# Performance work log

Measured on AMD Instinct MI355X. Metric: run time of the kernel, lower is better.

Reference implementation:

```python
import jax, jax.numpy as jnp
import numpy as np
from jax import lax

B, T, V, LAT, U, P = 256, 128, 42, 200, 512, 3  # batch, seq, vocab, latent, lstm units, num_prop


def setup_inputs() -> dict:
    key = jax.random.key(0)
    ks = jax.random.split(key, 40)
    g = lambda i, shape, s=0.05: (jax.random.normal(ks[i], shape, jnp.float32) * s)
    inp = {
        'X': jax.random.randint(ks[0], (B, T), 0, V, jnp.int64 if jax.config.jax_enable_x64 else jnp.int32),
        'Y': jax.random.randint(ks[1], (B, T), 0, V, jnp.int32),
        'C': jax.random.normal(ks[2], (B, P), jnp.float32),
        'L': jax.random.randint(ks[3], (B,), 1, T + 1, jnp.int32),
        'eps': jax.random.normal(ks[4], (B, LAT), jnp.float32),
        'emb_enc': g(5, (V, LAT), 0.1),
        'emb_dec': g(6, (V, LAT), 0.1),
        # encoder stacked LSTM: layer0 input dim = LAT + P, layers 1-2 input dim = U
        'enc_k0': g(7, (LAT + P, 4 * U)), 'enc_rk0': g(8, (U, 4 * U)), 'enc_b0': jnp.zeros((4 * U,), jnp.float32),
        'enc_k1': g(9, (U, 4 * U)), 'enc_rk1': g(10, (U, 4 * U)), 'enc_b1': jnp.zeros((4 * U,), jnp.float32),
        'enc_k2': g(11, (U, 4 * U)), 'enc_rk2': g(12, (U, 4 * U)), 'enc_b2': jnp.zeros((4 * U,), jnp.float32),
        # decoder stacked LSTM: layer0 input dim = 2*LAT + P
        'dec_k0': g(13, (2 * LAT + P, 4 * U)), 'dec_rk0': g(14, (U, 4 * U)), 'dec_b0': jnp.zeros((4 * U,), jnp.float32),
        'dec_k1': g(15, (U, 4 * U)), 'dec_rk1': g(16, (U, 4 * U)), 'dec_b1': jnp.zeros((4 * U,), jnp.float32),
        'dec_k2': g(17, (U, 4 * U)), 'dec_rk2': g(18, (U, 4 * U)), 'dec_b2': jnp.zeros((4 * U,), jnp.float32),
        'Wm': g(19, (U, LAT)), 'bm': jnp.zeros((LAT,), jnp.float32),
        'Ws': g(20, (U, LAT)), 'bs': jnp.zeros((LAT,), jnp.float32),
        'Wo': g(21, (U, V)), 'bo': jnp.zeros((V,), jnp.float32),
    }
    return inp


def _lstm_step(x, h, c, k, rk, b):
    # Keras LSTMCell gate order: i, f, g(candidate), o
    z = x @ k + h @ rk + b
    i, f, gg, o = jnp.split(z, 4, axis=-1)
    c2 = jax.nn.sigmoid(f) * c + jax.nn.sigmoid(i) * jnp.tanh(gg)
    h2 = jax.nn.sigmoid(o) * jnp.tanh(c2)
    return h2, c2


def _run_stacked(inp, params):
    # inp: [B, T, D]; params: list of 3 (kernel, recurrent_kernel, bias)
    b = inp.shape[0]
    init = tuple((jnp.zeros((b, U), inp.dtype), jnp.zeros((b, U), inp.dtype)) for _ in range(3))

    def scan_fn(carry, x_t):
        h_in = x_t
        new = []
        for (h, c), (k, rk, bb) in zip(carry, params):
            h2, c2 = _lstm_step(h_in, h, c, k, rk, bb)
            new.append((h2, c2))
            h_in = h2
        return tuple(new), h_in

    carry, ys = lax.scan(scan_fn, init, jnp.swapaxes(inp, 0, 1))
    return jnp.swapaxes(ys, 0, 1), carry  # [B,T,U], final states


def reference(X, Y, C, L, eps, emb_enc, emb_dec,
              enc_k0, enc_rk0, enc_b0, enc_k1, enc_rk1, enc_b1, enc_k2, enc_rk2, enc_b2,
              dec_k0, dec_rk0, dec_b0, dec_k1, dec_rk1, dec_b1, dec_k2, dec_rk2, dec_b2,
              Wm, bm, Ws, bs, Wo, bo):
    enc_params = [(enc_k0, enc_rk0, enc_b0), (enc_k1, enc_rk1, enc_b1), (enc_k2, enc_rk2, enc_b2)]
    dec_params = [(dec_k0, dec_rk0, dec_b0), (dec_k1, dec_rk1, dec_b1), (dec_k2, dec_rk2, dec_b2)]

    # ---- encode ----
    Xe = emb_enc[X]                                       # [B,T,LAT]
    Ct = jnp.broadcast_to(C[:, None, :], (B, T, P))
    enc_in = jnp.concatenate([Xe, Ct], axis=-1)           # [B,T,LAT+P]
    _, enc_states = _run_stacked(enc_in, enc_params)
    h = enc_states[-1][1]                                 # CELL state of last layer (state[-1][1])
    mean = h @ Wm + bm
    log_sigma = h @ Ws + bs
    z = mean + jnp.exp(log_sigma / 2.0) * eps             # [B,LAT]

    # ---- decode ----
    Zt = jnp.broadcast_to(z[:, None, :], (B, T, LAT))
    Xd = emb_dec[X]
    dec_in = jnp.concatenate([Zt, Xd, Ct], axis=-1)       # [B,T,2*LAT+P]
    dec_out, _ = _run_stacked(dec_in, dec_params)
    pre = dec_out @ Wo + bo                               # pre-softmax logits [B,T,V]

    # ---- losses ----
    logp = jax.nn.log_softmax(pre, axis=-1)
    ce = -jnp.take_along_axis(logp, Y[..., None].astype(jnp.int32), axis=-1)[..., 0]  # [B,T]
    weights = (jnp.arange(T)[None, :] < L[:, None]).astype(jnp.float32)
    recon = jnp.mean(ce * weights)
    latent = -0.5 * jnp.mean(1.0 + log_sigma - jnp.square(mean) - jnp.exp(log_sigma))
    loss = recon + latent
    return loss, recon, latent
```

## Files before the change

### kernel.cpp

```cpp
#include <hip/hip_runtime.h>

#define B_ 256
#define T_ 128
#define V_ 42
#define LAT_ 200
#define U_ 512
#define G4_ 2048
#define NBLK 196
#define FI(r, m) ((((r) * 2) + (m)) * 32)
#define SLOT_ ((size_t)B_ * U_)
#define LS_ ((size_t)129 * SLOT_)

typedef unsigned short ushort_t;
typedef __attribute__((ext_vector_type(8))) short bf8;
typedef __attribute__((ext_vector_type(4))) float f4;

__device__ __forceinline__ ushort_t f2bf(float f) {
  union { float f; unsigned int i; } v; v.f = f;
  unsigned int r = v.i + 0x7fffu + ((v.i >> 16) & 1u);
  return (ushort_t)(r >> 16);
}
__device__ __forceinline__ float sigf(float x) { return 1.f / (1.f + __expf(-x)); }
__device__ __forceinline__ float tanhfast(float x) {
  float e = __expf(2.f * x);
  return 1.f - 2.f / (e + 1.f);
}

__device__ __forceinline__ void st_wt_b16(void* p, ushort_t v) {
  unsigned int vv = v;
  asm volatile("global_store_short %0, %1, off sc0 sc1" :: "v"(p), "v"(vv) : "memory");
}
__device__ __forceinline__ void st_wt_b32(void* p, unsigned int v) {
  asm volatile("global_store_dword %0, %1, off sc0 sc1" :: "v"(p), "v"(v) : "memory");
}
__device__ __forceinline__ void wait_vm0() {
  asm volatile("s_waitcnt vmcnt(0)" ::: "memory");
}

__global__ __launch_bounds__(256) void table_kernel(const float* emb, const float* k0, int roff, float* table) {
  int v = blockIdx.x, tid = threadIdx.x;
  __shared__ float e[LAT_];
  for (int i = tid; i < LAT_; i += 256) e[i] = emb[v * LAT_ + i];
  __syncthreads();
  for (int j = tid; j < G4_; j += 256) {
    float s = 0.f;
    for (int n = 0; n < LAT_; n++) s += e[n] * k0[(size_t)(roff + n) * G4_ + j];
    table[v * G4_ + j] = s;
  }
}

__device__ __forceinline__ size_t mat_off_u4(int m) {
  if (m == 0) return 0;
  if (m == 1) return 147456;
  if (m < 10) return 360448 + (size_t)(m - 2) * 131072;
  return 1409024;
}

struct SwzSrc {
  const float *enc_rk0, *enc_k0, *enc_b0;
  const float *dec_rk0, *dec_k0, *dec_b0;
  const float *tabE, *tabD;
  const float *encK1, *encR1, *encK2, *encR2;
  const float *decK1, *decR1, *decK2, *decR2;
  const float *Wo;
  ushort_t* dst;
};

__device__ float swz_val(const SwzSrc& s, int mat, int k, int n) {
  switch (mat) {
    case 0: {
      if (k < 512) return s.enc_rk0[(size_t)k * G4_ + n];
      int i = k - 512;
      if (i < 42) return s.tabE[(size_t)i * G4_ + n];
      if (i < 45) return s.enc_k0[(size_t)(200 + i - 42) * G4_ + n];
      if (i == 45) return s.enc_b0[n];
      return 0.f;
    }
    case 1: {
      if (k < 512) return s.dec_rk0[(size_t)k * G4_ + n];
      int i = k - 512;
      if (i < 200) return s.dec_k0[(size_t)i * G4_ + n];
      if (i < 256) return 0.f;
      i -= 256;
      if (i < 42) return s.tabD[(size_t)i * G4_ + n];
      if (i < 45) return s.dec_k0[(size_t)(400 + i - 42) * G4_ + n];
      if (i == 45) return s.dec_b0[n];
      return 0.f;
    }
    case 2: return s.encK1[(size_t)k * G4_ + n];
    case 3: return s.encR1[(size_t)k * G4_ + n];
    case 4: return s.encK2[(size_t)k * G4_ + n];
    case 5: return s.encR2[(size_t)k * G4_ + n];
    case 6: return s.decK1[(size_t)k * G4_ + n];
    case 7: return s.decR1[(size_t)k * G4_ + n];
    case 8: return s.decK2[(size_t)k * G4_ + n];
    case 9: return s.decR2[(size_t)k * G4_ + n];
    default: return (n < V_) ? s.Wo[(size_t)k * V_ + n] : 0.f;
  }
}

__global__ __launch_bounds__(256) void swz_ext_kernel(SwzSrc s) {
  int b = blockIdx.x, tid = threadIdx.x;
  int mat, nt16;
  if (b < 1280) { mat = b >> 7; nt16 = b & 127; } else { mat = 10; nt16 = b - 1280; }
  int ktMax = (mat == 0) ? 18 : (mat == 1) ? 26 : 16;
  int lane = tid & 63, l15 = lane & 15, q = lane >> 4;
  int n = nt16 * 16 + l15;
  uint4* dst = (uint4*)s.dst;
  size_t off = mat_off_u4(mat);
  for (int kt = tid >> 6; kt < ktMax; kt += 4) {
    ushort_t o[8];
    int kb = kt * 32 + q * 8;
#pragma unroll
    for (int j = 0; j < 8; j++) o[j] = f2bf(swz_val(s, mat, kb + j, n));
    dst[off + ((size_t)nt16 * ktMax + kt) * 64 + lane] = *(const uint4*)o;
  }
}

struct PP {
  const ushort_t* swz;
  ushort_t* ring;
  float* c2g; ushort_t* zf16; float* sums; int* bar; int* gen; int* flg; float* out;
  const float *enc_b1, *enc_b2, *dec_b1, *dec_b2;
  const float *Wm, *bm, *Ws, *bs, *eps, *C, *bo;
  const int *X, *Y, *Lb;
};

__device__ __forceinline__ void grid_barrier(int* bar, int* gen) {
  __builtin_amdgcn_fence(__ATOMIC_RELEASE, "agent");
  __syncthreads();
  if (threadIdx.x == 0) {
    int g = __hip_atomic_load(gen, __ATOMIC_RELAXED, __HIP_MEMORY_SCOPE_AGENT);
    if (__hip_atomic_fetch_add(bar, 1, __ATOMIC_ACQ_REL, __HIP_MEMORY_SCOPE_AGENT) == NBLK - 1) {
      __hip_atomic_store(bar, 0, __ATOMIC_RELAXED, __HIP_MEMORY_SCOPE_AGENT);
      __hip_atomic_store(gen, g + 1, __ATOMIC_RELEASE, __HIP_MEMORY_SCOPE_AGENT);
    } else {
      int gg;
      do {
        __builtin_amdgcn_s_sleep(1);
        gg = __hip_atomic_load(gen, __ATOMIC_ACQUIRE, __HIP_MEMORY_SCOPE_AGENT);
      } while (gg == g);
    }
  }
  __syncthreads();
  __builtin_amdgcn_fence(__ATOMIC_ACQUIRE, "agent");
}

__device__ __forceinline__ void wait_flags(const int* f, int cnt, int target) {
  int lane = threadIdx.x & 63;
  const int* a = f + (lane < cnt ? lane : 0);
  bool bad;
  do {
    int v = __hip_atomic_load(a, __ATOMIC_RELAXED, __HIP_MEMORY_SCOPE_AGENT);
    bad = (lane < cnt) && (v < target);
    if (__ballot(bad) == 0ull) break;
    __builtin_amdgcn_s_sleep(1);
  } while (true);
}

#define MFMA(a, bfrag, c) __builtin_amdgcn_mfma_f32_16x16x32_bf16((a), (bfrag), (c), 0, 0, 0)

__global__ __launch_bounds__(256, 1) void persist(PP p) {
  __shared__ uint4 wlds4[8192];
  const int b = blockIdx.x, tid = threadIdx.x;
  const int lane = tid & 63, w = tid >> 6, q = lane >> 4, l15 = lane & 15;
  const int role = b < 64 ? 0 : b < 128 ? 1 : b < 192 ? 2 : 3;
  const int idx = b & 63;
  const int ut = idx >> 1;
  const int mi = idx & 1;
  const int m0 = mi * 128;
  const int rw = m0 + w * 32;
  const int u = ut * 16 + l15;
  const uint4* swzU4 = (const uint4*)p.swz;
  const int cb = b - 192;

  unsigned char* tok = (unsigned char*)wlds4 + 106496;
  unsigned char* ytok = (unsigned char*)wlds4 + 49152;

  ushort_t cb0[2][3];
  if (role == 0) {
#pragma unroll
    for (int ms = 0; ms < 2; ms++)
#pragma unroll
      for (int j = 0; j < 3; j++) cb0[ms][j] = f2bf(p.C[(rw + ms * 16 + l15) * 3 + j]);
  }

  const int pubidx = FI(role, mi) + ut;

  float ce_local = 0.f;
  float boR0 = 0.f, boR1 = 0.f, boR2 = 0.f;
  int Lr[4] = {0, 0, 0, 0};
  int pub = 0;

  for (int phase = 0; phase < 2; phase++) {
    const bool dec = (phase == 1);

    if (dec) {
      grid_barrier(p.bar, p.gen);
      if (b < 50) {
        int lat0 = b * 4;
        int row = tid;
        float m[4], ls[4];
#pragma unroll
        for (int lc = 0; lc < 4; lc++) { m[lc] = p.bm[lat0 + lc]; ls[lc] = p.bs[lat0 + lc]; }
        const float* cr = p.c2g + (size_t)row * U_;
        for (int k = 0; k < U_; k++) {
          float hv = cr[k];
#pragma unroll
          for (int lc = 0; lc < 4; lc++) {
            m[lc] += hv * p.Wm[k * LAT_ + lat0 + lc];
            ls[lc] += hv * p.Ws[k * LAT_ + lat0 + lc];
          }
        }
        float kl = 0.f;
#pragma unroll
        for (int lc = 0; lc < 4; lc++) {
          int lat = lat0 + lc;
          float zz = m[lc] + __expf(0.5f * ls[lc]) * p.eps[row * LAT_ + lat];
          p.zf16[row * 256 + lat] = f2bf(zz);
          kl += 1.f + ls[lc] - m[lc] * m[lc] - __expf(ls[lc]);
        }
        float* red = (float*)wlds4;
        red[tid] = kl; __syncthreads();
        for (int st = 128; st > 0; st >>= 1) { if (tid < st) red[tid] += red[tid + st]; __syncthreads(); }
        if (tid == 0) atomicAdd(p.sums + 1, red[0]);
      }
      __syncthreads();
    }

    const int KT = dec ? 26 : 18;
    if (role == 0) {
      int mat = dec ? 1 : 0;
      size_t mo = mat_off_u4(mat);
      for (int g = 0; g < 4; g++) {
        int nt16 = g * 32 + ut;
        size_t src = mo + (size_t)nt16 * KT * 64;
        int dst = g * KT * 64;
        for (int i = tid; i < KT * 64; i += 256) wlds4[dst + i] = swzU4[src + i];
      }
      if (!dec) {
        for (int i = tid; i < 128 * T_; i += 256) {
          int r = i >> 7, t = i & 127;
          tok[r * 133 + t] = (unsigned char)p.X[(size_t)(m0 + r) * T_ + t];
        }
      }
    } else if (role <= 2) {
      int matK = dec ? (role == 1 ? 6 : 8) : (role == 1 ? 2 : 4);
      for (int gm = 0; gm < 2; gm++) {
        size_t mo = mat_off_u4(matK + gm);
        for (int g = 0; g < 4; g++) {
          int nt16 = g * 32 + ut;
          size_t src = mo + (size_t)nt16 * 1024;
          int dst = gm * 4096 + g * 1024;
          for (int i = tid; i < 1024; i += 256) wlds4[dst + i] = swzU4[src + i];
        }
      }
    } else if (dec) {
      size_t mo = mat_off_u4(10);
      for (int i = tid; i < 3072; i += 256) wlds4[i] = swzU4[mo + i];
      for (int i = tid; i < 64 * T_; i += 256) {
        int r = i >> 7, t = i & 127;
        ytok[r * 133 + t] = (unsigned char)p.Y[(size_t)(cb * 64 + r) * T_ + t];
      }
      int r0c = cb * 64 + w * 16;
      boR0 = p.bo[l15]; boR1 = p.bo[16 + l15]; boR2 = (l15 < 10) ? p.bo[32 + l15] : 0.f;
#pragma unroll
      for (int r = 0; r < 4; r++) Lr[r] = p.Lb[r0c + q * 4 + r];
    }
    __syncthreads();

    float creg[2][4];
#pragma unroll
    for (int ms = 0; ms < 2; ms++)
#pragma unroll
      for (int r = 0; r < 4; r++) creg[ms][r] = 0.f;
    float bias[4] = {0.f, 0.f, 0.f, 0.f};
    if (role == 1 || role == 2) {
      const float* bb = dec ? (role == 1 ? p.dec_b1 : p.dec_b2) : (role == 1 ? p.enc_b1 : p.enc_b2);
#pragma unroll
      for (int g = 0; g < 4; g++) bias[g] = bb[g * 512 + u];
    }

    const int* myp = nullptr; int myc = 0;
    if (role == 0) {
      if (w == 0) { myp = p.flg + FI(0, mi); myc = 32; }
    } else if (role == 1) {
      if (w == 0) { myp = p.flg + FI(0, mi); myc = 32; }
      else if (w == 1) { myp = p.flg + FI(1, mi); myc = 32; }
    } else if (role == 2) {
      if (w == 0) { myp = p.flg + FI(1, mi); myc = 32; }
      else if (w == 1) { myp = p.flg + FI(2, mi); myc = 32; }
    } else {
      if (w == 0 && dec) { myp = p.flg + FI(2, cb >> 1); myc = 32; }
    }

    grid_barrier(p.bar, p.gen);

    bf8 zr0[8], zr1[8];
    if (role == 0 && dec) {
      const ushort_t* Az0 = p.zf16 + (rw + l15) * 256 + q * 8;
#pragma unroll
      for (int kz = 0; kz < 8; kz++) {
        zr0[kz] = *(const bf8*)(Az0 + kz * 32);
        zr1[kz] = *(const bf8*)(Az0 + 16 * 256 + kz * 32);
      }
    }

    const int smax = dec ? T_ + 3 : T_ + 2;
    for (int s = 0; s < smax; s++) {
      pub++;
      if (myc) wait_flags(myp, myc, pub - 1);
      __syncthreads();

      const int lag = (role <= 2) ? role : 3;
      const int t = s - lag;
      if (role == 3) {
        if (dec && t >= 0 && t < T_) {
          int r0c = cb * 64 + w * 16;
          const ushort_t* Ar = p.ring + 2 * LS_ + (size_t)(t + 1) * SLOT_ + (size_t)(r0c + l15) * U_ + q * 8;
          f4 a3[3];
#pragma unroll
          for (int nt = 0; nt < 3; nt++) a3[nt] = (f4){0.f, 0.f, 0.f, 0.f};
#pragma unroll 4
          for (int kt = 0; kt < 16; kt++) {
            bf8 a = *(const bf8*)(Ar + kt * 32);
#pragma unroll
            for (int nt = 0; nt < 3; nt++) {
              bf8 bbf = *(const bf8*)&wlds4[nt * 1024 + kt * 64 + lane];
              a3[nt] = MFMA(a, bbf, a3[nt]);
            }
          }
#pragma unroll
          for (int r = 0; r < 4; r++) {
            float v0 = a3[0][r] + boR0;
            float v1 = a3[1][r] + boR1;
            float v2 = (l15 < 10) ? a3[2][r] + boR2 : -3.0e38f;
            float mx = fmaxf(fmaxf(v0, v1), v2);
            mx = fmaxf(mx, __shfl_xor(mx, 1)); mx = fmaxf(mx, __shfl_xor(mx, 2));
            mx = fmaxf(mx, __shfl_xor(mx, 4)); mx = fmaxf(mx, __shfl_xor(mx, 8));
            float se = __expf(v0 - mx) + __expf(v1 - mx) + ((l15 < 10) ? __expf(v2 - mx) : 0.f);
            int yv = ytok[(w * 16 + q * 4 + r) * 133 + t];
            float py = (l15 == yv ? v0 : 0.f) + (l15 + 16 == yv ? v1 : 0.f) + (l15 + 32 == yv ? v2 : 0.f);
            se += __shfl_xor(se, 1); se += __shfl_xor(se, 2); se += __shfl_xor(se, 4); se += __shfl_xor(se, 8);
            py += __shfl_xor(py, 1); py += __shfl_xor(py, 2); py += __shfl_xor(py, 4); py += __shfl_xor(py, 8);
            if (l15 == 0 && t < Lr[r]) ce_local += mx + __logf(se) - py;
          }
        }
      } else if (t >= 0 && t < T_) {
        f4 acc[2][4];
#pragma unroll
        for (int ms = 0; ms < 2; ms++)
#pragma unroll
          for (int g = 0; g < 4; g++) acc[ms][g] = (f4){0.f, 0.f, 0.f, 0.f};

        const ushort_t* hin = p.ring + (size_t)role * LS_ + (size_t)t * SLOT_;
        ushort_t* hout = p.ring + (size_t)role * LS_ + (size_t)(t + 1) * SLOT_;
        const ushort_t* Ah0 = hin + (size_t)(rw + l15) * U_ + q * 8;
        const ushort_t* Ah1 = Ah0 + 16 * U_;

        if (role == 0) {
          const int KT64 = KT * 64;
#pragma unroll 4
          for (int kt = 0; kt < 16; kt++) {
            bf8 a0 = *(const bf8*)(Ah0 + kt * 32);
            bf8 a1 = *(const bf8*)(Ah1 + kt * 32);
#pragma unroll
            for (int g = 0; g < 4; g++) {
              bf8 bbf = *(const bf8*)&wlds4[g * KT64 + kt * 64 + lane];
              acc[0][g] = MFMA(a0, bbf, acc[0][g]);
              acc[1][g] = MFMA(a1, bbf, acc[1][g]);
            }
          }
          if (dec) {
#pragma unroll
            for (int kz = 0; kz < 8; kz++) {
#pragma unroll
              for (int g = 0; g < 4; g++) {
                bf8 bbf = *(const bf8*)&wlds4[g * KT64 + (16 + kz) * 64 + lane];
                acc[0][g] = MFMA(zr0[kz], bbf, acc[0][g]);
                acc[1][g] = MFMA(zr1[kz], bbf, acc[1][g]);
              }
            }
          }
          int xv0 = tok[(w * 32 + l15) * 133 + t];
          int xv1 = tok[(w * 32 + 16 + l15) * 133 + t];
#pragma unroll
          for (int ktc = 0; ktc < 2; ktc++) {
            union { ushort_t us[8]; bf8 v; } a0u, a1u;
#pragma unroll
            for (int j = 0; j < 8; j++) {
              int id = ktc * 32 + q * 8 + j;
              ushort_t v0 = (id == xv0) ? (ushort_t)0x3F80 : (ushort_t)0;
              ushort_t v1 = (id == xv1) ? (ushort_t)0x3F80 : (ushort_t)0;
              if (id >= 42 && id < 45) { v0 = cb0[0][id - 42]; v1 = cb0[1][id - 42]; }
              if (id == 45) { v0 = 0x3F80; v1 = 0x3F80; }
              a0u.us[j] = v0; a1u.us[j] = v1;
            }
            int kt = KT - 2 + ktc;
#pragma unroll
            for (int g = 0; g < 4; g++) {
              bf8 bbf = *(const bf8*)&wlds4[g * KT64 + kt * 64 + lane];
              acc[0][g] = MFMA(a0u.v, bbf, acc[0][g]);
              acc[1][g] = MFMA(a1u.v, bbf, acc[1][g]);
            }
          }
        } else {
          const ushort_t* xin = p.ring + (size_t)(role - 1) * LS_ + (size_t)(t + 1) * SLOT_;
          const ushort_t* Ax0 = xin + (size_t)(rw + l15) * U_ + q * 8;
          const ushort_t* Ax1 = Ax0 + 16 * U_;
#pragma unroll 4
          for (int kt = 0; kt < 16; kt++) {
            bf8 a0 = *(const bf8*)(Ax0 + kt * 32);
            bf8 a1 = *(const bf8*)(Ax1 + kt * 32);
#pragma unroll
            for (int g = 0; g < 4; g++) {
              bf8 bbf = *(const bf8*)&wlds4[g * 1024 + kt * 64 + lane];
              acc[0][g] = MFMA(a0, bbf, acc[0][g]);
              acc[1][g] = MFMA(a1, bbf, acc[1][g]);
            }
          }
#pragma unroll 4
          for (int kt = 0; kt < 16; kt++) {
            bf8 a0 = *(const bf8*)(Ah0 + kt * 32);
            bf8 a1 = *(const bf8*)(Ah1 + kt * 32);
#pragma unroll
            for (int g = 0; g < 4; g++) {
              bf8 bbf = *(const bf8*)&wlds4[4096 + g * 1024 + kt * 64 + lane];
              acc[0][g] = MFMA(a0, bbf, acc[0][g]);
              acc[1][g] = MFMA(a1, bbf, acc[1][g]);
            }
          }
        }

#pragma unroll
        for (int ms = 0; ms < 2; ms++)
#pragma unroll
          for (int r = 0; r < 4; r++) {
            int row = rw + ms * 16 + q * 4 + r;
            float zi = acc[ms][0][r] + bias[0];
            float zf = acc[ms][1][r] + bias[1];
            float zg = acc[ms][2][r] + bias[2];
            float zo = acc[ms][3][r] + bias[3];
            float cp = creg[ms][r];
            float cn = sigf(zf) * cp + sigf(zi) * tanhfast(zg);
            float hn = sigf(zo) * tanhfast(cn);
            creg[ms][r] = cn;
            st_wt_b16(&hout[(size_t)row * U_ + u], f2bf(hn));
            if (!dec && role == 2 && t == T_ - 1) p.c2g[(size_t)row * U_ + u] = cn;
          }
      }
      wait_vm0();
      __syncthreads();
      if (tid == 0 && role < 3) st_wt_b32(p.flg + pubidx, (unsigned int)pub);
    }
  }

  if (role == 3 && l15 == 0) atomicAdd(p.sums + 0, ce_local);
  grid_barrier(p.bar, p.gen);
  if (b == 0 && tid == 0) {
    float recon = p.sums[0] * (1.f / ((float)B_ * (float)T_));
    float latent = -0.5f * p.sums[1] * (1.f / ((float)B_ * (float)LAT_));
    p.out[0] = recon + latent;
    p.out[1] = recon;
    p.out[2] = latent;
  }
}

extern "C" void kernel_launch(void* const* d_in, const int* in_sizes, int n_in,
                              void* d_out, int out_size, void* d_ws, size_t ws_size,
                              hipStream_t stream) {
  const int*   X       = (const int*)d_in[0];
  const int*   Y       = (const int*)d_in[1];
  const float* C       = (const float*)d_in[2];
  const int*   L       = (const int*)d_in[3];
  const float* eps     = (const float*)d_in[4];
  const float* emb_enc = (const float*)d_in[5];
  const float* emb_dec = (const float*)d_in[6];
  const float* enc_k0  = (const float*)d_in[7];
  const float* enc_rk0 = (const float*)d_in[8];
  const float* enc_b0  = (const float*)d_in[9];
  const float* enc_k1  = (const float*)d_in[10];
  const float* enc_rk1 = (const float*)d_in[11];
  const float* enc_b1  = (const float*)d_in[12];
  const float* enc_k2  = (const float*)d_in[13];
  const float* enc_rk2 = (const float*)d_in[14];
  const float* enc_b2  = (const float*)d_in[15];
  const float* dec_k0  = (const float*)d_in[16];
  const float* dec_rk0 = (const float*)d_in[17];
  const float* dec_b0  = (const float*)d_in[18];
  const float* dec_k1  = (const float*)d_in[19];
  const float* dec_rk1 = (const float*)d_in[20];
  const float* dec_b1  = (const float*)d_in[21];
  const float* dec_k2  = (const float*)d_in[22];
  const float* dec_rk2 = (const float*)d_in[23];
  const float* dec_b2  = (const float*)d_in[24];
  const float* Wm      = (const float*)d_in[25];
  const float* bm      = (const float*)d_in[26];
  const float* Ws      = (const float*)d_in[27];
  const float* bs      = (const float*)d_in[28];
  const float* Wo      = (const float*)d_in[29];
  const float* bo      = (const float*)d_in[30];
  float* out = (float*)d_out;
  (void)in_sizes; (void)n_in; (void)out_size; (void)ws_size;

  char* wsb = (char*)d_ws;
  size_t o = 0;
  auto take = [&](size_t bytes) -> char* { char* p = wsb + o; o += (bytes + 255) & ~(size_t)255; return p; };

  float* c2g  = (float*)take((size_t)B_ * U_ * 4);
  ushort_t* zf16 = (ushort_t*)take((size_t)B_ * 256 * 2);
  float* sums = (float*)take(8);
  int* bar = (int*)take(4);
  int* gen = (int*)take(4);
  int* flg = (int*)take(4 * 2 * 32 * 4);
  size_t zero_bytes = o;
  ushort_t* ring = (ushort_t*)take(3 * LS_ * 2);
  ushort_t* swz = (ushort_t*)take((size_t)1412096 * 16);
  float* tabE = (float*)take((size_t)V_ * G4_ * 4);
  float* tabD = (float*)take((size_t)V_ * G4_ * 4);

  hipMemsetAsync(wsb, 0, zero_bytes, stream);
  for (int l = 0; l < 3; l++)
    hipMemsetAsync(ring + (size_t)l * LS_, 0, SLOT_ * 2, stream);

  table_kernel<<<V_, 256, 0, stream>>>(emb_enc, enc_k0, 0, tabE);
  table_kernel<<<V_, 256, 0, stream>>>(emb_dec, dec_k0, 200, tabD);

  SwzSrc ss;
  ss.enc_rk0 = enc_rk0; ss.enc_k0 = enc_k0; ss.enc_b0 = enc_b0;
  ss.dec_rk0 = dec_rk0; ss.dec_k0 = dec_k0; ss.dec_b0 = dec_b0;
  ss.tabE = tabE; ss.tabD = tabD;
  ss.encK1 = enc_k1; ss.encR1 = enc_rk1; ss.encK2 = enc_k2; ss.encR2 = enc_rk2;
  ss.decK1 = dec_k1; ss.decR1 = dec_rk1; ss.decK2 = dec_k2; ss.decR2 = dec_rk2;
  ss.Wo = Wo; ss.dst = swz;
  swz_ext_kernel<<<1283, 256, 0, stream>>>(ss);

  PP pp;
  pp.swz = swz; pp.ring = ring;
  pp.c2g = c2g; pp.zf16 = zf16; pp.sums = sums; pp.bar = bar; pp.gen = gen; pp.flg = flg; pp.out = out;
  pp.enc_b1 = enc_b1; pp.enc_b2 = enc_b2; pp.dec_b1 = dec_b1; pp.dec_b2 = dec_b2;
  pp.Wm = Wm; pp.bm = bm; pp.Ws = Ws; pp.bs = bs; pp.eps = eps; pp.C = C; pp.bo = bo;
  pp.X = X; pp.Y = Y; pp.Lb = L;
  persist<<<NBLK, 256, 0, stream>>>(pp);
}
```

Measured before the change: 5.007 ms.

## Hoist constant z-projection out of decoder loop, pack h stores, spin without sleep

In the decoder's first layer, the contribution of the latent z to the gate pre-activations does not change across timesteps. It is now computed once before the time loop and used as the starting accumulator, which removes 64 MFMAs per step on the critical recurrent path. The LDS weight layout is reorganised so the z weights sit in a separate region. The hidden-state writes now pack pairs of bf16 values via a lane shuffle and store them with 32-bit relaxed atomic exchanges in place of the write-through short stores, and the flag-wait loop drops its s_sleep. Busier spinning adds memory traffic, and the visibility of atomic exchange relative to the old sc0/sc1 stores has to hold for correctness.

```diff
diff --git a/kernel.cpp b/kernel.cpp
--- a/kernel.cpp
+++ b/kernel.cpp
@@ -24,14 +24,6 @@
 __device__ __forceinline__ float tanhfast(float x) {
   float e = __expf(2.f * x);
   return 1.f - 2.f / (e + 1.f);
-}
-
-__device__ __forceinline__ void st_wt_b16(void* p, ushort_t v) {
-  unsigned int vv = v;
-  asm volatile("global_store_short %0, %1, off sc0 sc1" :: "v"(p), "v"(vv) : "memory");
-}
-__device__ __forceinline__ void st_wt_b32(void* p, unsigned int v) {
-  asm volatile("global_store_dword %0, %1, off sc0 sc1" :: "v"(p), "v"(v) : "memory");
 }
 __device__ __forceinline__ void wait_vm0() {
   asm volatile("s_waitcnt vmcnt(0)" ::: "memory");
@@ -153,9 +145,7 @@
   do {
     int v = __hip_atomic_load(a, __ATOMIC_RELAXED, __HIP_MEMORY_SCOPE_AGENT);
     bad = (lane < cnt) && (v < target);
-    if (__ballot(bad) == 0ull) break;
-    __builtin_amdgcn_s_sleep(1);
-  } while (true);
+  } while (__ballot(bad) != 0ull);
 }
 
 #define MFMA(a, bfrag, c) __builtin_amdgcn_mfma_f32_16x16x32_bf16((a), (bfrag), (c), 0, 0, 0)
@@ -228,20 +218,28 @@
       __syncthreads();
     }
 
-    const int KT = dec ? 26 : 18;
     if (role == 0) {
-      int mat = dec ? 1 : 0;
-      size_t mo = mat_off_u4(mat);
-      for (int g = 0; g < 4; g++) {
-        int nt16 = g * 32 + ut;
-        size_t src = mo + (size_t)nt16 * KT * 64;
-        int dst = g * KT * 64;
-        for (int i = tid; i < KT * 64; i += 256) wlds4[dst + i] = swzU4[src + i];
-      }
       if (!dec) {
+        size_t mo = mat_off_u4(0);
+        for (int g = 0; g < 4; g++) {
+          int nt16 = g * 32 + ut;
+          size_t src = mo + (size_t)nt16 * 18 * 64;
+          int dst = g * 18 * 64;
+          for (int i = tid; i < 18 * 64; i += 256) wlds4[dst + i] = swzU4[src + i];
+        }
         for (int i = tid; i < 128 * T_; i += 256) {
           int r = i >> 7, t = i & 127;
           tok[r * 133 + t] = (unsigned char)p.X[(size_t)(m0 + r) * T_ + t];
+        }
+      } else {
+        size_t mo = mat_off_u4(1);
+        for (int g = 0; g < 4; g++) {
+          int nt16 = g * 32 + ut;
+          size_t src = mo + (size_t)nt16 * 26 * 64;
+          int dst = g * 18 * 64;
+          for (int i = tid; i < 16 * 64; i += 256) wlds4[dst + i] = swzU4[src + i];
+          for (int i = tid; i < 2 * 64; i += 256) wlds4[dst + 16 * 64 + i] = swzU4[src + 24 * 64 + i];
+          for (int i = tid; i < 8 * 64; i += 256) wlds4[4608 + g * 512 + i] = swzU4[src + 16 * 64 + i];
         }
       }
     } else if (role <= 2) {
@@ -296,13 +294,23 @@
 
     grid_barrier(p.bar, p.gen);
 
-    bf8 zr0[8], zr1[8];
+    f4 zacc[2][4];
+#pragma unroll
+    for (int ms = 0; ms < 2; ms++)
+#pragma unroll
+      for (int g = 0; g < 4; g++) zacc[ms][g] = (f4){0.f, 0.f, 0.f, 0.f};
     if (role == 0 && dec) {
       const ushort_t* Az0 = p.zf16 + (rw + l15) * 256 + q * 8;
 #pragma unroll
       for (int kz = 0; kz < 8; kz++) {
-        zr0[kz] = *(const bf8*)(Az0 + kz * 32);
-        zr1[kz] = *(const bf8*)(Az0 + 16 * 256 + kz * 32);
+        bf8 a0 = *(const bf8*)(Az0 + kz * 32);
+        bf8 a1 = *(const bf8*)(Az0 + 16 * 256 + kz * 32);
+#pragma unroll
+        for (int g = 0; g < 4; g++) {
+          bf8 bbf = *(const bf8*)&wlds4[4608 + g * 512 + kz * 64 + lane];
+          zacc[0][g] = MFMA(a0, bbf, zacc[0][g]);
+          zacc[1][g] = MFMA(a1, bbf, zacc[1][g]);
+        }
       }
     }
 
@@ -351,7 +359,7 @@
 #pragma unroll
         for (int ms = 0; ms < 2; ms++)
 #pragma unroll
-          for (int g = 0; g < 4; g++) acc[ms][g] = (f4){0.f, 0.f, 0.f, 0.f};
+          for (int g = 0; g < 4; g++) acc[ms][g] = zacc[ms][g];
 
         const ushort_t* hin = p.ring + (size_t)role * LS_ + (size_t)t * SLOT_;
         ushort_t* hout = p.ring + (size_t)role * LS_ + (size_t)(t + 1) * SLOT_;
@@ -359,7 +367,7 @@
         const ushort_t* Ah1 = Ah0 + 16 * U_;
 
         if (role == 0) {
-          const int KT64 = KT * 64;
+          const int KT64 = 18 * 64;
 #pragma unroll 4
           for (int kt = 0; kt < 16; kt++) {
             bf8 a0 = *(const bf8*)(Ah0 + kt * 32);
@@ -369,17 +377,6 @@
               bf8 bbf = *(const bf8*)&wlds4[g * KT64 + kt * 64 + lane];
               acc[0][g] = MFMA(a0, bbf, acc[0][g]);
               acc[1][g] = MFMA(a1, bbf, acc[1][g]);
-            }
-          }
-          if (dec) {
-#pragma unroll
-            for (int kz = 0; kz < 8; kz++) {
-#pragma unroll
-              for (int g = 0; g < 4; g++) {
-                bf8 bbf = *(const bf8*)&wlds4[g * KT64 + (16 + kz) * 64 + lane];
-                acc[0][g] = MFMA(zr0[kz], bbf, acc[0][g]);
-                acc[1][g] = MFMA(zr1[kz], bbf, acc[1][g]);
-              }
             }
           }
           int xv0 = tok[(w * 32 + l15) * 133 + t];
@@ -396,7 +393,7 @@
               if (id == 45) { v0 = 0x3F80; v1 = 0x3F80; }
               a0u.us[j] = v0; a1u.us[j] = v1;
             }
-            int kt = KT - 2 + ktc;
+            int kt = 16 + ktc;
 #pragma unroll
             for (int g = 0; g < 4; g++) {
               bf8 bbf = *(const bf8*)&wlds4[g * KT64 + kt * 64 + lane];
@@ -445,13 +442,20 @@
             float cn = sigf(zf) * cp + sigf(zi) * tanhfast(zg);
             float hn = sigf(zo) * tanhfast(cn);
             creg[ms][r] = cn;
-            st_wt_b16(&hout[(size_t)row * U_ + u], f2bf(hn));
+            unsigned int part = (unsigned int)f2bf(hn);
+            unsigned int up = (unsigned int)__shfl_xor((int)part, 1);
+            if ((l15 & 1) == 0) {
+              unsigned int packed = part | (up << 16);
+              __hip_atomic_exchange((unsigned int*)&hout[(size_t)row * U_ + u], packed,
+                                    __ATOMIC_RELAXED, __HIP_MEMORY_SCOPE_AGENT);
+            }
             if (!dec && role == 2 && t == T_ - 1) p.c2g[(size_t)row * U_ + u] = cn;
           }
       }
       wait_vm0();
       __syncthreads();
-      if (tid == 0 && role < 3) st_wt_b32(p.flg + pubidx, (unsigned int)pub);
+      if (tid == 0 && role < 3)
+        __hip_atomic_exchange(p.flg + pubidx, pub, __ATOMIC_RELAXED, __HIP_MEMORY_SCOPE_AGENT);
     }
   }
 
```

Measured after the change: 5.086 ms. Within noise of the previous version (+1.6%).
